# Optimization experiments

Hardware: AMD Instinct MI355X
Metric: run time of the kernel (lower is better)

## Reference

```python
import jax, jax.numpy as jnp
import numpy as np

B, T, D, H = 2, 2048, 1024, 16
DK = D // H  # 64


def setup_inputs() -> dict:
    key = jax.random.key(0)
    ks = jax.random.split(key, 13)
    s = 1.0 / np.sqrt(D)
    return {
        "x": jax.random.normal(ks[0], (B, T, D), jnp.float32),
        "Wq_w": jax.random.normal(ks[1], (D, D), jnp.float32) * s,
        "Wq_b": jax.random.normal(ks[2], (D,), jnp.float32) * 0.01,
        "Wk_w": jax.random.normal(ks[3], (D, D), jnp.float32) * s,
        "Wk_b": jax.random.normal(ks[4], (D,), jnp.float32) * 0.01,
        "Wv_w": jax.random.normal(ks[5], (D, D), jnp.float32) * s,
        "Wv_b": jax.random.normal(ks[6], (D,), jnp.float32) * 0.01,
        "Wo_w": jax.random.normal(ks[7], (D, D), jnp.float32) * s,
        "Wo_b": jax.random.normal(ks[8], (D,), jnp.float32) * 0.01,
        "qr": jax.random.normal(ks[9], (B, H, T, DK), jnp.float32),
        "qi": jax.random.normal(ks[10], (B, H, T, DK), jnp.float32),
        "kr": jax.random.normal(ks[11], (B, H, T, DK), jnp.float32),
        "ki": jax.random.normal(ks[12], (B, H, T, DK), jnp.float32),
    }


def _heads(y):
    # [B,T,D] -> [B,H,T,DK]
    return y.reshape(B, T, H, DK).transpose(0, 2, 1, 3)


def reference(x, Wq_w, Wq_b, Wk_w, Wk_b, Wv_w, Wv_b, Wo_w, Wo_b, qr, qi, kr, ki):
    Q = _heads(x @ Wq_w.T + Wq_b)
    K = _heads(x @ Wk_w.T + Wk_b)
    V = _heads(x @ Wv_w.T + Wv_b)
    # quantum noise: sin(atan2(imag, real))
    Q = Q + jnp.sin(jnp.arctan2(qi, qr))
    K = K + jnp.sin(jnp.arctan2(ki, kr))
    # Recursive fractal attention collapses: branches are identical and
    # deterministic, so (A1+A2)/2 == depth-0 attention at every level.
    scores = jnp.einsum("bhtd,bhsd->bhts", Q, K) / np.sqrt(DK).astype(np.float32)
    weights = jax.nn.softmax(scores, axis=-1)
    attn = jnp.einsum("bhts,bhsd->bhtd", weights, V)  # [B,H,T,DK]
    out = attn.transpose(0, 2, 1, 3).reshape(B, T, D)
    return out @ Wo_w.T + Wo_b
```

## Files before the change

kernel.cpp:

```cpp
#include <hip/hip_runtime.h>
#include <hip/hip_fp16.h>
#include <stdint.h>

typedef _Float16 half_t;
typedef _Float16 hf2 __attribute__((ext_vector_type(2)));
typedef _Float16 hf4 __attribute__((ext_vector_type(4)));
typedef _Float16 hf8 __attribute__((ext_vector_type(8)));
typedef float f32x16 __attribute__((ext_vector_type(16)));
typedef unsigned uint2_t __attribute__((ext_vector_type(2)));

#define LOG2E 1.4426950408889634f

__device__ __forceinline__ void gload16(const void* g, void* l) {
  __builtin_amdgcn_global_load_lds(
      (const __attribute__((address_space(1))) unsigned int*)g,
      (__attribute__((address_space(3))) unsigned int*)l, 16, 0, 0);
}

__device__ __forceinline__ unsigned packrtz(float a, float b) {
  auto h = __builtin_amdgcn_cvt_pkrtz(a, b);
  union { decltype(h) h2; unsigned u; } c;
  c.h2 = h;
  return c.u;
}

__device__ __forceinline__ float exp2fast(float x) {
#if __has_builtin(__builtin_amdgcn_exp2f)
  return __builtin_amdgcn_exp2f(x);
#else
  return exp2f(x);
#endif
}

__device__ __forceinline__ float psum2(unsigned pw, hf2 ones, float acc) {
#if __has_builtin(__builtin_amdgcn_fdot2)
  union { unsigned u; hf2 h; } c;
  c.u = pw;
  return __builtin_amdgcn_fdot2(c.h, ones, acc, false);
#else
  union { unsigned u; hf2 h; } c;
  c.u = pw;
  return acc + (float)c.h[0] + (float)c.h[1];
#endif
}

__global__ __launch_bounds__(256) void cvt_kernel(
    const float* __restrict__ x, const float* __restrict__ wq,
    const float* __restrict__ wk, const float* __restrict__ wv,
    const float* __restrict__ wo, half_t* __restrict__ xh,
    half_t* __restrict__ wh) {
  long e = ((long)blockIdx.x * 256 + threadIdx.x) * 16;
  const float* src;
  half_t* dst;
  if (e < 4194304L) {
    src = x + e;
    dst = xh + e;
  } else {
    long j = e - 4194304L;
    int w = (int)(j >> 20);
    long off = j & 1048575L;
    src = (w == 0 ? wq : w == 1 ? wk : w == 2 ? wv : wo) + off;
    dst = wh + ((long)w << 20) + off;
  }
  const float4* s4 = (const float4*)src;
  float4 f0 = s4[0], f1 = s4[1], f2 = s4[2], f3 = s4[3];
  hf8 o0 = {(half_t)f0.x, (half_t)f0.y, (half_t)f0.z, (half_t)f0.w,
            (half_t)f1.x, (half_t)f1.y, (half_t)f1.z, (half_t)f1.w};
  hf8 o1 = {(half_t)f2.x, (half_t)f2.y, (half_t)f2.z, (half_t)f2.w,
            (half_t)f3.x, (half_t)f3.y, (half_t)f3.z, (half_t)f3.w};
  *(hf8*)dst = o0;
  *(hf8*)(dst + 8) = o1;
}

__device__ __forceinline__ void gemm_core(const half_t* __restrict__ A,
                                          const half_t* __restrict__ Bt,
                                          int m0, int n0, char* ldsb,
                                          f32x16 acc[2]) {
  const int tid = threadIdx.x;
  const int wid = tid >> 6;
  const int lane = tid & 63;
  const int l31 = lane & 31;
  const int hh = lane >> 5;
  const int wm = wid >> 1, wn = wid & 1;

#pragma unroll
  for (int mt = 0; mt < 2; mt++)
#pragma unroll
    for (int i = 0; i < 16; i++) acc[mt][i] = 0.f;

  const int rowb = tid >> 3;
  const int c16 = (tid & 7) ^ (rowb & 7);
  int goA = (m0 + rowb) * 1024 + c16 * 8;
  int goB = (n0 + rowb) * 1024 + c16 * 8;

  const int swz0 = (hh * 16) ^ ((l31 & 7) << 4);
  const int swz1 = (32 + hh * 16) ^ ((l31 & 7) << 4);
  const int swz2 = (64 + hh * 16) ^ ((l31 & 7) << 4);
  const int swz3 = (96 + hh * 16) ^ ((l31 & 7) << 4);
  const int arow = (wm * 64 + l31) * 128;
  const int brow = 16384 + (wn * 32 + l31) * 128;
  const int aof0 = arow + swz0, aof1 = arow + swz1, aof2 = arow + swz2,
            aof3 = arow + swz3;
  const int bof0 = brow + swz0, bof1 = brow + swz1, bof2 = brow + swz2,
            bof3 = brow + swz3;

  for (int kt = 0; kt < 16; ++kt) {
#pragma unroll
    for (int i = 0; i < 4; i++)
      gload16(A + goA + i * 32768, ldsb + i * 4096 + wid * 1024);
#pragma unroll
    for (int i = 0; i < 2; i++)
      gload16(Bt + goB + i * 32768, ldsb + 16384 + i * 4096 + wid * 1024);
    goA += 64;
    goB += 64;
    __syncthreads();
#pragma unroll
    for (int kc = 0; kc < 4; kc++) {
      const int ao = (kc == 0 ? aof0 : kc == 1 ? aof1 : kc == 2 ? aof2 : aof3);
      const int bo = (kc == 0 ? bof0 : kc == 1 ? bof1 : kc == 2 ? bof2 : bof3);
      hf8 af0 = *(const hf8*)(ldsb + ao);
      hf8 af1 = *(const hf8*)(ldsb + ao + 4096);
      hf8 bf = *(const hf8*)(ldsb + bo);
      acc[0] = __builtin_amdgcn_mfma_f32_32x32x16_f16(af0, bf, acc[0], 0, 0, 0);
      acc[1] = __builtin_amdgcn_mfma_f32_32x32x16_f16(af1, bf, acc[1], 0, 0, 0);
    }
    __syncthreads();
  }
}

__global__ __launch_bounds__(256, 4) void proj_kernel(
    const half_t* __restrict__ xh, const half_t* __restrict__ wh,
    const float* __restrict__ bq, const float* __restrict__ bk,
    const float* __restrict__ bv, const float* __restrict__ qr,
    const float* __restrict__ qi, const float* __restrict__ kr,
    const float* __restrict__ ki, half_t* __restrict__ Qh,
    half_t* __restrict__ Kh, half_t* __restrict__ Vth) {
  __shared__ __align__(16) char ldsb[24576];
  const int z = blockIdx.z;
  const half_t* Bt = wh + (size_t)z * 1048576;
  const int m0 = blockIdx.x * 128, n0 = blockIdx.y * 64;
  f32x16 acc[2];
  gemm_core(xh, Bt, m0, n0, ldsb, acc);

  const int tid = threadIdx.x;
  const int wid = tid >> 6;
  const int lane = tid & 63;
  const int l31 = lane & 31;
  const int hh = lane >> 5;
  const int wm = wid >> 1, wn = wid & 1;
  const float* bias = (z == 0) ? bq : (z == 1) ? bk : bv;
  const float* nr = (z == 0) ? qr : kr;
  const float* ni = (z == 0) ? qi : ki;
  const float scale = (z == 0) ? (0.125f * LOG2E) : 1.0f;

  const int n = n0 + wn * 32 + l31;
  const float bsv = bias[n];
  const int hd = n >> 6, d = n & 63;
#pragma unroll
  for (int mt = 0; mt < 2; mt++) {
    const int mbase = m0 + wm * 64 + mt * 32;
    if (z == 2) {
#pragma unroll
      for (int g = 0; g < 4; g++) {
        const int m = mbase + 8 * g + 4 * hh;
        const int bb = m >> 11, tt = m & 2047;
        hf4 pk;
#pragma unroll
        for (int i2 = 0; i2 < 4; i2++)
          pk[i2] = (half_t)(acc[mt][4 * g + i2] + bsv);
        *(hf4*)(Vth + (((size_t)(bb * 16 + hd) * 64 + d) * 2048 + tt)) = pk;
      }
    } else {
      half_t* dstp = (z == 0) ? Qh : Kh;
#pragma unroll
      for (int r = 0; r < 16; r++) {
        const int m = mbase + (r & 3) + 8 * (r >> 2) + 4 * hh;
        const int bb = m >> 11, tt = m & 2047;
        const size_t idx = ((size_t)(bb * 16 + hd) * 2048 + tt) * 64 + d;
        float v = acc[mt][r] + bsv;
        const float a_ = nr[idx], b_ = ni[idx];
        v += b_ * rsqrtf(a_ * a_ + b_ * b_);
        dstp[idx] = (half_t)(v * scale);
      }
    }
  }
}

template <int CUR>
__device__ __forceinline__ void attn_tile_t(
    bool stage, const half_t* __restrict__ Kb, const half_t* __restrict__ Vb,
    char* base, int qw, int& gk0, int& gk1, int& gv0, int& gv1,
    const int kofs[4], const hf8 qf[4], const f32x16& zv, f32x16 ot[2],
    float& psAcc, hf2 ones) {
  if (stage) {
    gload16(Kb + gk0, base + (CUR ^ 1) * 8192 + qw * 1024);
    gload16(Kb + gk1, base + (CUR ^ 1) * 8192 + 4096 + qw * 1024);
    gload16(Vb + gv0, base + 16384 + (CUR ^ 1) * 8192 + qw * 1024);
    gload16(Vb + gv1, base + 16384 + (CUR ^ 1) * 8192 + 4096 + qw * 1024);
    gk0 += 4096;
    gk1 += 4096;
    gv0 += 64;
    gv1 += 64;
  }
#pragma unroll
  for (int kt = 0; kt < 2; kt++) {
    __builtin_amdgcn_s_setprio(1);
    f32x16 s = __builtin_amdgcn_mfma_f32_32x32x16_f16(
        *(const hf8*)(base + kofs[0] + CUR * 8192 + kt * 4096), qf[0], zv, 0, 0,
        0);
    s = __builtin_amdgcn_mfma_f32_32x32x16_f16(
        *(const hf8*)(base + kofs[1] + CUR * 8192 + kt * 4096), qf[1], s, 0, 0,
        0);
    s = __builtin_amdgcn_mfma_f32_32x32x16_f16(
        *(const hf8*)(base + kofs[2] + CUR * 8192 + kt * 4096), qf[2], s, 0, 0,
        0);
    s = __builtin_amdgcn_mfma_f32_32x32x16_f16(
        *(const hf8*)(base + kofs[3] + CUR * 8192 + kt * 4096), qf[3], s, 0, 0,
        0);
    __builtin_amdgcn_s_setprio(0);

    unsigned pw[8];
#pragma unroll
    for (int j = 0; j < 8; j++) {
      float p0 = exp2fast(s[2 * j]);
      float p1 = exp2fast(s[2 * j + 1]);
      pw[j] = packrtz(p0, p1);
      psAcc = psum2(pw[j], ones, psAcc);
    }

#pragma unroll
    for (int sub = 0; sub < 2; sub++) {
      const int kc = kt * 2 + sub;
      unsigned a0 = pw[sub * 4 + 0], a1 = pw[sub * 4 + 1];
      unsigned a2 = pw[sub * 4 + 2], a3 = pw[sub * 4 + 3];
      union { unsigned u[4]; hf8 v; } pu;
#if __has_builtin(__builtin_amdgcn_permlane32_swap)
      uint2_t r02 = __builtin_amdgcn_permlane32_swap(a0, a2, false, false);
      uint2_t r13 = __builtin_amdgcn_permlane32_swap(a1, a3, false, false);
      pu.u[0] = r02[0];
      pu.u[1] = r13[0];
      pu.u[2] = r02[1];
      pu.u[3] = r13[1];
#else
      const int hh_ = (threadIdx.x & 63) >> 5;
      unsigned x0 = __shfl_xor(a0, 32, 64), x1 = __shfl_xor(a1, 32, 64);
      unsigned x2 = __shfl_xor(a2, 32, 64), x3 = __shfl_xor(a3, 32, 64);
      pu.u[0] = hh_ ? x2 : a0;
      pu.u[1] = hh_ ? x3 : a1;
      pu.u[2] = hh_ ? a2 : x0;
      pu.u[3] = hh_ ? a3 : x1;
#endif
      __builtin_amdgcn_s_setprio(1);
#pragma unroll
      for (int dt = 0; dt < 2; dt++) {
        hf8 vf =
            *(const hf8*)(base + kofs[kc] + 16384 + CUR * 8192 + dt * 4096);
        ot[dt] =
            __builtin_amdgcn_mfma_f32_32x32x16_f16(vf, pu.v, ot[dt], 0, 0, 0);
      }
      __builtin_amdgcn_s_setprio(0);
    }
  }
  __syncthreads();
}

__global__ __launch_bounds__(512, 4) void attn_kernel(
    const half_t* __restrict__ Qh, const half_t* __restrict__ Kh,
    const half_t* __restrict__ Vth, half_t* __restrict__ ah) {
  __shared__ __align__(16) char smem[65536];
  const int tid = threadIdx.x, wid = tid >> 6, lane = tid & 63;
  const int l31 = lane & 31, hh = lane >> 5;
  const int qw = wid & 3, g = wid >> 2;
  const int lin = blockIdx.x;
  const int slot = lin >> 3;
  const int bh = (lin & 7) * 4 + (slot >> 4);
  const int qb = slot & 15;
  const int b = bh >> 4, hd = bh & 15;
  const int t = qb * 128 + qw * 32 + l31;

  char* base = smem + g * 32768;

  const half_t* qrow = Qh + ((size_t)bh * 2048 + t) * 64;
  hf8 qf[4];
#pragma unroll
  for (int kc = 0; kc < 4; kc++) qf[kc] = *(const hf8*)(qrow + kc * 16 + hh * 8);

  f32x16 ot[2];
#pragma unroll
  for (int dt = 0; dt < 2; dt++)
#pragma unroll
    for (int i = 0; i < 16; i++) ot[dt][i] = 0.f;
  f32x16 zv;
#pragma unroll
  for (int i = 0; i < 16; i++) zv[i] = 0.f;
  float psAcc = 0.f;
  const hf2 ones = {(_Float16)1.0f, (_Float16)1.0f};

  const half_t* Kb = Kh + (size_t)bh * 2048 * 64;
  const half_t* Vb = Vth + (size_t)bh * 64 * 2048;
  const int kvbase = g * 1024;

  int kofs[4];
#pragma unroll
  for (int kc = 0; kc < 4; kc++)
    kofs[kc] = l31 * 128 + ((kc * 32 + hh * 16) ^ ((l31 & 7) << 4));

  int gk0, gk1, gv0, gv1;
  {
    int c0 = qw * 64 + lane, c1 = 256 + qw * 64 + lane;
    int r0 = c0 >> 3, s0 = (c0 & 7) ^ (r0 & 7);
    int r1 = c1 >> 3, s1 = (c1 & 7) ^ (r1 & 7);
    gk0 = (kvbase + r0) * 64 + s0 * 8;
    gk1 = (kvbase + r1) * 64 + s1 * 8;
    gv0 = r0 * 2048 + kvbase + s0 * 8;
    gv1 = r1 * 2048 + kvbase + s1 * 8;
  }
  gload16(Kb + gk0, base + qw * 1024);
  gload16(Kb + gk1, base + 4096 + qw * 1024);
  gload16(Vb + gv0, base + 16384 + qw * 1024);
  gload16(Vb + gv1, base + 16384 + 4096 + qw * 1024);
  gk0 += 4096;
  gk1 += 4096;
  gv0 += 64;
  gv1 += 64;
  __syncthreads();

  for (int tp = 0; tp < 8; ++tp) {
    attn_tile_t<0>(true, Kb, Vb, base, qw, gk0, gk1, gv0, gv1, kofs, qf, zv,
                   ot, psAcc, ones);
    attn_tile_t<1>(tp < 7, Kb, Vb, base, qw, gk0, gk1, gv0, gv1, kofs, qf, zv,
                   ot, psAcc, ones);
  }

  const float lrun = psAcc + __shfl_xor(psAcc, 32, 64);

  float* cb = (float*)smem;
  float* lb = (float*)(smem + 32768);
  if (g == 1) {
#pragma unroll
    for (int dt = 0; dt < 2; dt++)
#pragma unroll
      for (int i = 0; i < 16; i++)
        cb[((qw * 2 + dt) * 16 + i) * 64 + lane] = ot[dt][i];
    lb[qw * 64 + lane] = lrun;
  }
  __syncthreads();
  if (g == 0) {
#pragma unroll
    for (int dt = 0; dt < 2; dt++)
#pragma unroll
      for (int i = 0; i < 16; i++)
        ot[dt][i] += cb[((qw * 2 + dt) * 16 + i) * 64 + lane];
    const float inv = 1.0f / (lrun + lb[qw * 64 + lane]);
    const size_t obase = ((size_t)b * 2048 + t) * 1024 + hd * 64;
#pragma unroll
    for (int dt = 0; dt < 2; dt++)
#pragma unroll
      for (int gg = 0; gg < 4; gg++) {
        hf4 pk;
#pragma unroll
        for (int i2 = 0; i2 < 4; i2++)
          pk[i2] = (half_t)(ot[dt][4 * gg + i2] * inv);
        *(hf4*)(ah + obase + dt * 32 + 8 * gg + 4 * hh) = pk;
      }
  }
}

__global__ __launch_bounds__(256, 4) void outproj_kernel(
    const half_t* __restrict__ ah, const half_t* __restrict__ woh,
    const float* __restrict__ bo, float* __restrict__ out) {
  __shared__ __align__(16) char ldsb[24576];
  const int m0 = blockIdx.x * 128, n0 = blockIdx.y * 64;
  f32x16 acc[2];
  gemm_core(ah, woh, m0, n0, ldsb, acc);
  const int tid = threadIdx.x, wid = tid >> 6, lane = tid & 63;
  const int l31 = lane & 31, hh = lane >> 5;
  const int wm = wid >> 1, wn = wid & 1;
  const int n = n0 + wn * 32 + l31;
  const float bsv = bo[n];
#pragma unroll
  for (int mt = 0; mt < 2; mt++) {
    const int mbase = m0 + wm * 64 + mt * 32;
#pragma unroll
    for (int r = 0; r < 16; r++) {
      const int m = mbase + (r & 3) + 8 * (r >> 2) + 4 * hh;
      out[(size_t)m * 1024 + n] = acc[mt][r] + bsv;
    }
  }
}

extern "C" void kernel_launch(void* const* d_in, const int* in_sizes, int n_in,
                              void* d_out, int out_size, void* d_ws,
                              size_t ws_size, hipStream_t stream) {
  const float* x = (const float*)d_in[0];
  const float* Wq = (const float*)d_in[1];
  const float* bq = (const float*)d_in[2];
  const float* Wk = (const float*)d_in[3];
  const float* bk = (const float*)d_in[4];
  const float* Wv = (const float*)d_in[5];
  const float* bv = (const float*)d_in[6];
  const float* Wo = (const float*)d_in[7];
  const float* bo = (const float*)d_in[8];
  const float* qr = (const float*)d_in[9];
  const float* qi = (const float*)d_in[10];
  const float* kr = (const float*)d_in[11];
  const float* ki = (const float*)d_in[12];
  float* out = (float*)d_out;

  char* ws = (char*)d_ws;
  half_t* xh = (half_t*)(ws);
  half_t* wh = (half_t*)(ws + 8388608);
  half_t* Qh = (half_t*)(ws + 16777216);
  half_t* Kh = (half_t*)(ws + 25165824);
  half_t* Vth = (half_t*)(ws + 33554432);
  half_t* ah = (half_t*)(ws + 41943040);

  cvt_kernel<<<dim3(2048), dim3(256), 0, stream>>>(x, Wq, Wk, Wv, Wo, xh, wh);
  proj_kernel<<<dim3(32, 16, 3), dim3(256), 0, stream>>>(
      xh, wh, bq, bk, bv, qr, qi, kr, ki, Qh, Kh, Vth);
  attn_kernel<<<dim3(512), dim3(512), 0, stream>>>(Qh, Kh, Vth, ah);
  outproj_kernel<<<dim3(32, 16), dim3(256), 0, stream>>>(ah, wh + 3 * 1048576,
                                                         bo, out);
}
```

Before: 113.5 us.

## Double-buffer LDS tiles in shared GEMM core to overlap loads with MFMA

```diff
diff --git a/kernel.cpp b/kernel.cpp
--- a/kernel.cpp
+++ b/kernel.cpp
@@ -72,6 +72,40 @@
   *(hf8*)(dst + 8) = o1;
 }
 
+template <int CUR>
+__device__ __forceinline__ void gstep(bool stage, const half_t* __restrict__ A,
+                                      const half_t* __restrict__ Bt, char* ldsb,
+                                      int wid, int& goA, int& goB, int aof0,
+                                      int aof1, int aof2, int aof3, int bof0,
+                                      int bof1, int bof2, int bof3,
+                                      f32x16 acc[2]) {
+  if (stage) {
+#pragma unroll
+    for (int i = 0; i < 4; i++)
+      gload16(A + goA + i * 32768,
+              ldsb + (CUR ^ 1) * 16384 + i * 4096 + wid * 1024);
+#pragma unroll
+    for (int i = 0; i < 2; i++)
+      gload16(Bt + goB + i * 32768,
+              ldsb + 32768 + (CUR ^ 1) * 8192 + i * 4096 + wid * 1024);
+    goA += 64;
+    goB += 64;
+  }
+  constexpr int ca = CUR * 16384;
+  constexpr int cb = 32768 + CUR * 8192;
+#pragma unroll
+  for (int kc = 0; kc < 4; kc++) {
+    const int ao = (kc == 0 ? aof0 : kc == 1 ? aof1 : kc == 2 ? aof2 : aof3);
+    const int bo = (kc == 0 ? bof0 : kc == 1 ? bof1 : kc == 2 ? bof2 : bof3);
+    hf8 af0 = *(const hf8*)(ldsb + ca + ao);
+    hf8 af1 = *(const hf8*)(ldsb + ca + ao + 4096);
+    hf8 bf = *(const hf8*)(ldsb + cb + bo);
+    acc[0] = __builtin_amdgcn_mfma_f32_32x32x16_f16(af0, bf, acc[0], 0, 0, 0);
+    acc[1] = __builtin_amdgcn_mfma_f32_32x32x16_f16(af1, bf, acc[1], 0, 0, 0);
+  }
+  __syncthreads();
+}
+
 __device__ __forceinline__ void gemm_core(const half_t* __restrict__ A,
                                           const half_t* __restrict__ Bt,
                                           int m0, int n0, char* ldsb,
@@ -98,44 +132,38 @@
   const int swz2 = (64 + hh * 16) ^ ((l31 & 7) << 4);
   const int swz3 = (96 + hh * 16) ^ ((l31 & 7) << 4);
   const int arow = (wm * 64 + l31) * 128;
-  const int brow = 16384 + (wn * 32 + l31) * 128;
+  const int brow = (wn * 32 + l31) * 128;
   const int aof0 = arow + swz0, aof1 = arow + swz1, aof2 = arow + swz2,
             aof3 = arow + swz3;
   const int bof0 = brow + swz0, bof1 = brow + swz1, bof2 = brow + swz2,
             bof3 = brow + swz3;
 
-  for (int kt = 0; kt < 16; ++kt) {
-#pragma unroll
-    for (int i = 0; i < 4; i++)
-      gload16(A + goA + i * 32768, ldsb + i * 4096 + wid * 1024);
-#pragma unroll
-    for (int i = 0; i < 2; i++)
-      gload16(Bt + goB + i * 32768, ldsb + 16384 + i * 4096 + wid * 1024);
-    goA += 64;
-    goB += 64;
-    __syncthreads();
-#pragma unroll
-    for (int kc = 0; kc < 4; kc++) {
-      const int ao = (kc == 0 ? aof0 : kc == 1 ? aof1 : kc == 2 ? aof2 : aof3);
-      const int bo = (kc == 0 ? bof0 : kc == 1 ? bof1 : kc == 2 ? bof2 : bof3);
-      hf8 af0 = *(const hf8*)(ldsb + ao);
-      hf8 af1 = *(const hf8*)(ldsb + ao + 4096);
-      hf8 bf = *(const hf8*)(ldsb + bo);
-      acc[0] = __builtin_amdgcn_mfma_f32_32x32x16_f16(af0, bf, acc[0], 0, 0, 0);
-      acc[1] = __builtin_amdgcn_mfma_f32_32x32x16_f16(af1, bf, acc[1], 0, 0, 0);
-    }
-    __syncthreads();
-  }
-}
-
-__global__ __launch_bounds__(256, 4) void proj_kernel(
+#pragma unroll
+  for (int i = 0; i < 4; i++)
+    gload16(A + goA + i * 32768, ldsb + i * 4096 + wid * 1024);
+#pragma unroll
+  for (int i = 0; i < 2; i++)
+    gload16(Bt + goB + i * 32768, ldsb + 32768 + i * 4096 + wid * 1024);
+  goA += 64;
+  goB += 64;
+  __syncthreads();
+
+  for (int kp = 0; kp < 8; ++kp) {
+    gstep<0>(true, A, Bt, ldsb, wid, goA, goB, aof0, aof1, aof2, aof3, bof0,
+             bof1, bof2, bof3, acc);
+    gstep<1>(kp < 7, A, Bt, ldsb, wid, goA, goB, aof0, aof1, aof2, aof3, bof0,
+             bof1, bof2, bof3, acc);
+  }
+}
+
+__global__ __launch_bounds__(256, 3) void proj_kernel(
     const half_t* __restrict__ xh, const half_t* __restrict__ wh,
     const float* __restrict__ bq, const float* __restrict__ bk,
     const float* __restrict__ bv, const float* __restrict__ qr,
     const float* __restrict__ qi, const float* __restrict__ kr,
     const float* __restrict__ ki, half_t* __restrict__ Qh,
     half_t* __restrict__ Kh, half_t* __restrict__ Vth) {
-  __shared__ __align__(16) char ldsb[24576];
+  __shared__ __align__(16) char ldsb[49152];
   const int z = blockIdx.z;
   const half_t* Bt = wh + (size_t)z * 1048576;
   const int m0 = blockIdx.x * 128, n0 = blockIdx.y * 64;
@@ -366,10 +394,10 @@
   }
 }
 
-__global__ __launch_bounds__(256, 4) void outproj_kernel(
+__global__ __launch_bounds__(256, 3) void outproj_kernel(
     const half_t* __restrict__ ah, const half_t* __restrict__ woh,
     const float* __restrict__ bo, float* __restrict__ out) {
-  __shared__ __align__(16) char ldsb[24576];
+  __shared__ __align__(16) char ldsb[49152];
   const int m0 = blockIdx.x * 128, n0 = blockIdx.y * 64;
   f32x16 acc[2];
   gemm_core(ah, woh, m0, n0, ldsb, acc);
```

Result: faster. 108.3 us (median of 2 runs) (-4.5%).

## Enlarge GEMM tiles to 128x128 using 16x16x32 MFMA with 4x4 per-wave fragments

Applied to the files above, without the earlier changes.

```diff
diff --git a/kernel.cpp b/kernel.cpp
--- a/kernel.cpp
+++ b/kernel.cpp
@@ -6,6 +6,7 @@
 typedef _Float16 hf2 __attribute__((ext_vector_type(2)));
 typedef _Float16 hf4 __attribute__((ext_vector_type(4)));
 typedef _Float16 hf8 __attribute__((ext_vector_type(8)));
+typedef float f32x4 __attribute__((ext_vector_type(4)));
 typedef float f32x16 __attribute__((ext_vector_type(16)));
 typedef unsigned uint2_t __attribute__((ext_vector_type(2)));
 
@@ -72,115 +73,129 @@
   *(hf8*)(dst + 8) = o1;
 }
 
-__device__ __forceinline__ void gemm_core(const half_t* __restrict__ A,
-                                          const half_t* __restrict__ Bt,
-                                          int m0, int n0, char* ldsb,
-                                          f32x16 acc[2]) {
+__device__ __forceinline__ void gemm_core16(const half_t* __restrict__ A,
+                                            const half_t* __restrict__ Bt,
+                                            int m0, int n0, char* ldsb,
+                                            f32x4 acc[4][4]) {
   const int tid = threadIdx.x;
   const int wid = tid >> 6;
   const int lane = tid & 63;
-  const int l31 = lane & 31;
-  const int hh = lane >> 5;
+  const int l15 = lane & 15;
+  const int l4 = lane >> 4;
   const int wm = wid >> 1, wn = wid & 1;
 
 #pragma unroll
-  for (int mt = 0; mt < 2; mt++)
-#pragma unroll
-    for (int i = 0; i < 16; i++) acc[mt][i] = 0.f;
+  for (int mi = 0; mi < 4; mi++)
+#pragma unroll
+    for (int ni = 0; ni < 4; ni++)
+#pragma unroll
+      for (int i = 0; i < 4; i++) acc[mi][ni][i] = 0.f;
 
   const int rowb = tid >> 3;
   const int c16 = (tid & 7) ^ (rowb & 7);
   int goA = (m0 + rowb) * 1024 + c16 * 8;
   int goB = (n0 + rowb) * 1024 + c16 * 8;
 
-  const int swz0 = (hh * 16) ^ ((l31 & 7) << 4);
-  const int swz1 = (32 + hh * 16) ^ ((l31 & 7) << 4);
-  const int swz2 = (64 + hh * 16) ^ ((l31 & 7) << 4);
-  const int swz3 = (96 + hh * 16) ^ ((l31 & 7) << 4);
-  const int arow = (wm * 64 + l31) * 128;
-  const int brow = 16384 + (wn * 32 + l31) * 128;
-  const int aof0 = arow + swz0, aof1 = arow + swz1, aof2 = arow + swz2,
-            aof3 = arow + swz3;
-  const int bof0 = brow + swz0, bof1 = brow + swz1, bof2 = brow + swz2,
-            bof3 = brow + swz3;
+  const int l7 = lane & 7;
+  const int arow = (wm * 64 + l15) * 128;
+  const int brow = 16384 + (wn * 64 + l15) * 128;
+  const int aks0 = arow + ((l4) ^ l7) * 16;
+  const int aks1 = arow + ((4 + l4) ^ l7) * 16;
+  const int bks0 = brow + ((l4) ^ l7) * 16;
+  const int bks1 = brow + ((4 + l4) ^ l7) * 16;
 
   for (int kt = 0; kt < 16; ++kt) {
 #pragma unroll
-    for (int i = 0; i < 4; i++)
+    for (int i = 0; i < 4; i++) {
       gload16(A + goA + i * 32768, ldsb + i * 4096 + wid * 1024);
-#pragma unroll
-    for (int i = 0; i < 2; i++)
       gload16(Bt + goB + i * 32768, ldsb + 16384 + i * 4096 + wid * 1024);
+    }
     goA += 64;
     goB += 64;
     __syncthreads();
 #pragma unroll
-    for (int kc = 0; kc < 4; kc++) {
-      const int ao = (kc == 0 ? aof0 : kc == 1 ? aof1 : kc == 2 ? aof2 : aof3);
-      const int bo = (kc == 0 ? bof0 : kc == 1 ? bof1 : kc == 2 ? bof2 : bof3);
-      hf8 af0 = *(const hf8*)(ldsb + ao);
-      hf8 af1 = *(const hf8*)(ldsb + ao + 4096);
-      hf8 bf = *(const hf8*)(ldsb + bo);
-      acc[0] = __builtin_amdgcn_mfma_f32_32x32x16_f16(af0, bf, acc[0], 0, 0, 0);
-      acc[1] = __builtin_amdgcn_mfma_f32_32x32x16_f16(af1, bf, acc[1], 0, 0, 0);
+    for (int ks = 0; ks < 2; ks++) {
+      const int ao = ks ? aks1 : aks0;
+      const int bo = ks ? bks1 : bks0;
+      hf8 af[4], bf[4];
+#pragma unroll
+      for (int mi = 0; mi < 4; mi++)
+        af[mi] = *(const hf8*)(ldsb + ao + mi * 2048);
+#pragma unroll
+      for (int ni = 0; ni < 4; ni++)
+        bf[ni] = *(const hf8*)(ldsb + bo + ni * 2048);
+#pragma unroll
+      for (int mi = 0; mi < 4; mi++)
+#pragma unroll
+        for (int ni = 0; ni < 4; ni++)
+          acc[mi][ni] = __builtin_amdgcn_mfma_f32_16x16x32_f16(
+              af[mi], bf[ni], acc[mi][ni], 0, 0, 0);
     }
     __syncthreads();
   }
 }
 
-__global__ __launch_bounds__(256, 4) void proj_kernel(
+__global__ __launch_bounds__(256, 3) void proj_kernel(
     const half_t* __restrict__ xh, const half_t* __restrict__ wh,
     const float* __restrict__ bq, const float* __restrict__ bk,
     const float* __restrict__ bv, const float* __restrict__ qr,
     const float* __restrict__ qi, const float* __restrict__ kr,
     const float* __restrict__ ki, half_t* __restrict__ Qh,
     half_t* __restrict__ Kh, half_t* __restrict__ Vth) {
-  __shared__ __align__(16) char ldsb[24576];
+  __shared__ __align__(16) char ldsb[32768];
   const int z = blockIdx.z;
   const half_t* Bt = wh + (size_t)z * 1048576;
-  const int m0 = blockIdx.x * 128, n0 = blockIdx.y * 64;
-  f32x16 acc[2];
-  gemm_core(xh, Bt, m0, n0, ldsb, acc);
+  const int m0 = blockIdx.x * 128, n0 = blockIdx.y * 128;
+  f32x4 acc[4][4];
+  gemm_core16(xh, Bt, m0, n0, ldsb, acc);
 
   const int tid = threadIdx.x;
   const int wid = tid >> 6;
   const int lane = tid & 63;
-  const int l31 = lane & 31;
-  const int hh = lane >> 5;
+  const int l15 = lane & 15;
+  const int l4 = lane >> 4;
   const int wm = wid >> 1, wn = wid & 1;
   const float* bias = (z == 0) ? bq : (z == 1) ? bk : bv;
   const float* nr = (z == 0) ? qr : kr;
-  const float* ni = (z == 0) ? qi : ki;
+  const float* ni_ = (z == 0) ? qi : ki;
   const float scale = (z == 0) ? (0.125f * LOG2E) : 1.0f;
 
-  const int n = n0 + wn * 32 + l31;
-  const float bsv = bias[n];
-  const int hd = n >> 6, d = n & 63;
-#pragma unroll
-  for (int mt = 0; mt < 2; mt++) {
-    const int mbase = m0 + wm * 64 + mt * 32;
-    if (z == 2) {
-#pragma unroll
-      for (int g = 0; g < 4; g++) {
-        const int m = mbase + 8 * g + 4 * hh;
-        const int bb = m >> 11, tt = m & 2047;
+  if (z == 2) {
+#pragma unroll
+    for (int mi = 0; mi < 4; mi++) {
+      const int tb = m0 + wm * 64 + mi * 16 + l4 * 4;
+      const int bb = tb >> 11, tt = tb & 2047;
+#pragma unroll
+      for (int ni = 0; ni < 4; ni++) {
+        const int n = n0 + wn * 64 + ni * 16 + l15;
+        const float bsv = bias[n];
+        const int hd = n >> 6, d = n & 63;
         hf4 pk;
 #pragma unroll
-        for (int i2 = 0; i2 < 4; i2++)
-          pk[i2] = (half_t)(acc[mt][4 * g + i2] + bsv);
+        for (int r = 0; r < 4; r++) pk[r] = (half_t)(acc[mi][ni][r] + bsv);
         *(hf4*)(Vth + (((size_t)(bb * 16 + hd) * 64 + d) * 2048 + tt)) = pk;
       }
-    } else {
-      half_t* dstp = (z == 0) ? Qh : Kh;
-#pragma unroll
-      for (int r = 0; r < 16; r++) {
-        const int m = mbase + (r & 3) + 8 * (r >> 2) + 4 * hh;
-        const int bb = m >> 11, tt = m & 2047;
-        const size_t idx = ((size_t)(bb * 16 + hd) * 2048 + tt) * 64 + d;
-        float v = acc[mt][r] + bsv;
-        const float a_ = nr[idx], b_ = ni[idx];
-        v += b_ * rsqrtf(a_ * a_ + b_ * b_);
-        dstp[idx] = (half_t)(v * scale);
+    }
+  } else {
+    half_t* dstp = (z == 0) ? Qh : Kh;
+#pragma unroll
+    for (int mi = 0; mi < 4; mi++) {
+      const int tb = m0 + wm * 64 + mi * 16 + l4 * 4;
+      const int bb = tb >> 11, tt = tb & 2047;
+#pragma unroll
+      for (int ni = 0; ni < 4; ni++) {
+        const int n = n0 + wn * 64 + ni * 16 + l15;
+        const float bsv = bias[n];
+        const int hd = n >> 6, d = n & 63;
+        const size_t ibase = ((size_t)(bb * 16 + hd) * 2048 + tt) * 64 + d;
+#pragma unroll
+        for (int r = 0; r < 4; r++) {
+          const size_t idx = ibase + (size_t)r * 64;
+          float v = acc[mi][ni][r] + bsv;
+          const float a_ = nr[idx], b_ = ni_[idx];
+          v += b_ * rsqrtf(a_ * a_ + b_ * b_);
+          dstp[idx] = (half_t)(v * scale);
+        }
       }
     }
   }
@@ -366,25 +381,26 @@
   }
 }
 
-__global__ __launch_bounds__(256, 4) void outproj_kernel(
+__global__ __launch_bounds__(256, 3) void outproj_kernel(
     const half_t* __restrict__ ah, const half_t* __restrict__ woh,
     const float* __restrict__ bo, float* __restrict__ out) {
-  __shared__ __align__(16) char ldsb[24576];
-  const int m0 = blockIdx.x * 128, n0 = blockIdx.y * 64;
-  f32x16 acc[2];
-  gemm_core(ah, woh, m0, n0, ldsb, acc);
+  __shared__ __align__(16) char ldsb[32768];
+  const int m0 = blockIdx.x * 128, n0 = blockIdx.y * 128;
+  f32x4 acc[4][4];
+  gemm_core16(ah, woh, m0, n0, ldsb, acc);
   const int tid = threadIdx.x, wid = tid >> 6, lane = tid & 63;
-  const int l31 = lane & 31, hh = lane >> 5;
+  const int l15 = lane & 15, l4 = lane >> 4;
   const int wm = wid >> 1, wn = wid & 1;
-  const int n = n0 + wn * 32 + l31;
-  const float bsv = bo[n];
-#pragma unroll
-  for (int mt = 0; mt < 2; mt++) {
-    const int mbase = m0 + wm * 64 + mt * 32;
-#pragma unroll
-    for (int r = 0; r < 16; r++) {
-      const int m = mbase + (r & 3) + 8 * (r >> 2) + 4 * hh;
-      out[(size_t)m * 1024 + n] = acc[mt][r] + bsv;
+#pragma unroll
+  for (int mi = 0; mi < 4; mi++) {
+    const int mb = m0 + wm * 64 + mi * 16 + l4 * 4;
+#pragma unroll
+    for (int ni = 0; ni < 4; ni++) {
+      const int n = n0 + wn * 64 + ni * 16 + l15;
+      const float bsv = bo[n];
+#pragma unroll
+      for (int r = 0; r < 4; r++)
+        out[(size_t)(mb + r) * 1024 + n] = acc[mi][ni][r] + bsv;
     }
   }
 }
@@ -416,9 +432,9 @@
   half_t* ah = (half_t*)(ws + 41943040);
 
   cvt_kernel<<<dim3(2048), dim3(256), 0, stream>>>(x, Wq, Wk, Wv, Wo, xh, wh);
-  proj_kernel<<<dim3(32, 16, 3), dim3(256), 0, stream>>>(
+  proj_kernel<<<dim3(32, 8, 3), dim3(256), 0, stream>>>(
       xh, wh, bq, bk, bv, qr, qi, kr, ki, Qh, Kh, Vth);
   attn_kernel<<<dim3(512), dim3(512), 0, stream>>>(Qh, Kh, Vth, ah);
-  outproj_kernel<<<dim3(32, 16), dim3(256), 0, stream>>>(ah, wh + 3 * 1048576,
-                                                         bo, out);
-}
+  outproj_kernel<<<dim3(32, 8), dim3(256), 0, stream>>>(ah, wh + 3 * 1048576,
+                                                        bo, out);
+}
```

New measurement: 110.2 us. -2.9%, faster.
